# Kernel optimization log

Measured on AMD Instinct MI355X. Metric: run time of the kernel, lower is better.

Reference implementation:

```python
import jax, jax.numpy as jnp
import numpy as np

EPS = 1e-20

def efficient_squash(s):
    # Efficient-CapsNet squash: (1 - 1/e^||s||) * s/||s||
    n = jnp.linalg.norm(s, axis=-1, keepdims=True)
    return (1.0 - 1.0 / (jnp.exp(n) + EPS)) * (s / (n + EPS))

def setup_inputs() -> dict:
    key = jax.random.key(0)
    k1, k2 = jax.random.split(key)
    B, N, D_in = 32, 2048, 16
    K, D_out = 32, 16
    x = jax.random.normal(k1, (B, N, D_in), dtype=jnp.float32)
    # he_normal fan_in = N * D_in * ... ; use simple scaled normal init
    w = jax.random.normal(k2, (K, N, D_in, D_out), dtype=jnp.float32) * 0.05
    b = jnp.zeros((K, N, 1), dtype=jnp.float32)
    return {"x": x, "w": w, "b": b}

def reference(x, w, b):
    D_out = w.shape[-1]
    # projection: [B,N,D_in] x [K,N,D_in,D_out] -> [B,K,N,D_out]
    u = jnp.einsum('bji,kjiz->bkjz', x, w)
    # agreement c_{bkj} = sum_{i,z} u_{bkjz} u_{bkiz} = <u_j, sum_i u_i>
    t = jnp.sum(u, axis=2)                      # [B,K,D_out]
    c = jnp.einsum('bkjz,bkz->bkj', u, t)[..., None]  # [B,K,N,1]
    c = c / jnp.sqrt(jnp.asarray(D_out, jnp.float32))
    c = jax.nn.softmax(c, axis=1)               # softmax over capsules K
    c = c + b                                   # broadcast [K,N,1]
    s = jnp.sum(u * c, axis=2)                  # [B,K,D_out]
    return efficient_squash(s)
```

## Files before the change

### kernel.cpp

```cpp
#include <hip/hip_runtime.h>

#define NN 2048
#define KK 32

#define WS_U     0
#define WS_TP2   67108864UL
#define WS_T     67633152UL
#define WS_SPART 67698688UL
#define WS_NEED  71892992UL

__device__ __forceinline__ float bf_lo(unsigned v) { return __uint_as_float(v << 16); }
__device__ __forceinline__ float bf_hi(unsigned v) { return __uint_as_float(v & 0xffff0000u); }
__device__ __forceinline__ unsigned pack_bf16(float a, float b) {
    unsigned ua = __float_as_uint(a), ub = __float_as_uint(b);
    return ((ua + 0x8000u) >> 16) | ((ub + 0x8000u) & 0xffff0000u);
}

__global__ __launch_bounds__(128)
void k1_u(const float* __restrict__ x, const float* __restrict__ w,
          unsigned* __restrict__ u_pk)
{
    const int tid = threadIdx.x;
    const int zq  = tid & 3;
    const int k   = tid >> 2;
    const int j   = blockIdx.x;

    const float4* w4 = reinterpret_cast<const float4*>(
        w + (((size_t)k * NN + j) * 16) * 16) + zq;
    float4 wr[16];
#pragma unroll
    for (int i = 0; i < 16; ++i) wr[i] = w4[i * 4];

    unsigned* __restrict__ ub = u_pk + (size_t)j * 8192 + k * 8 + zq * 2;
#pragma unroll 4
    for (int b = 0; b < 32; ++b) {
        const float* __restrict__ xr = x + ((size_t)b * NN + j) * 16;
        float xs[16];
#pragma unroll
        for (int i = 0; i < 16; ++i) xs[i] = xr[i];
        float4 acc = make_float4(0.f, 0.f, 0.f, 0.f);
#pragma unroll
        for (int i = 0; i < 16; ++i) {
            acc.x = fmaf(xs[i], wr[i].x, acc.x);
            acc.y = fmaf(xs[i], wr[i].y, acc.y);
            acc.z = fmaf(xs[i], wr[i].z, acc.z);
            acc.w = fmaf(xs[i], wr[i].w, acc.w);
        }
        uint2 o;
        o.x = pack_bf16(acc.x, acc.y);
        o.y = pack_bf16(acc.z, acc.w);
        *reinterpret_cast<uint2*>(ub + (size_t)b * 256) = o;
    }
}

__global__ __launch_bounds__(1024)
void k2a_tpart(const unsigned* __restrict__ u_pk, float* __restrict__ t_part2)
{
    __shared__ float red[16][64][8];
    const int tid  = threadIdx.x;
    const int js   = tid >> 6;
    const int sl64 = tid & 63;
    const int b    = blockIdx.x >> 3;
    const int slj  = blockIdx.x & 7;

    const uint4* up = reinterpret_cast<const uint4*>(u_pk)
                    + ((size_t)(slj * 256 + js) * 32 + b) * 64 + sl64;
    float a[8];
#pragma unroll
    for (int e = 0; e < 8; ++e) a[e] = 0.f;
#pragma unroll
    for (int it = 0; it < 16; ++it) {
        uint4 v = up[(size_t)it * (16 * 32 * 64)];
        a[0] += bf_lo(v.x); a[1] += bf_hi(v.x);
        a[2] += bf_lo(v.y); a[3] += bf_hi(v.y);
        a[4] += bf_lo(v.z); a[5] += bf_hi(v.z);
        a[6] += bf_lo(v.w); a[7] += bf_hi(v.w);
    }
#pragma unroll
    for (int e = 0; e < 8; ++e) red[js][sl64][e] = a[e];
    __syncthreads();
    if (tid < 512) {
        const int s = tid >> 3, e = tid & 7;
        float acc = 0.f;
#pragma unroll
        for (int r = 0; r < 16; ++r) acc += red[r][s][e];
        t_part2[((size_t)b * 8 + slj) * 512 + s * 8 + e] = acc;
    }
}

__global__ __launch_bounds__(256)
void k2a2_t(const float* __restrict__ t_part2, float* __restrict__ t)
{
    const int idx4 = blockIdx.x * 256 + threadIdx.x;
    const int b = idx4 >> 7, loc4 = idx4 & 127;
    const float4* p = reinterpret_cast<const float4*>(t_part2) + (size_t)b * 1024 + loc4;
    float4 s = make_float4(0.f, 0.f, 0.f, 0.f);
#pragma unroll
    for (int sl = 0; sl < 8; ++sl) {
        float4 v = p[sl * 128];
        s.x += v.x; s.y += v.y; s.z += v.z; s.w += v.w;
    }
    reinterpret_cast<float4*>(t)[idx4] = s;
}

__global__ __launch_bounds__(256)
void k2b_fused(const unsigned* __restrict__ u_pk, const float* __restrict__ t,
               const float* __restrict__ bias, float* __restrict__ s_part)
{
    __shared__ float lc_lds[32][33];
    __shared__ float s_lds[8][32][16];
    const int tid = threadIdx.x;
    const int k   = tid & 31;
    const int jl  = tid >> 5;
    const int b   = blockIdx.x >> 6;
    const int jc  = blockIdx.x & 63;

    float tr[16];
    const float4* tp = reinterpret_cast<const float4*>(t + ((size_t)b * KK + k) * 16);
#pragma unroll
    for (int q = 0; q < 4; ++q) {
        float4 v = tp[q];
        tr[4 * q + 0] = v.x; tr[4 * q + 1] = v.y; tr[4 * q + 2] = v.z; tr[4 * q + 3] = v.w;
    }

    uint4 ua[4], ud[4];
#pragma unroll
    for (int jj = 0; jj < 4; ++jj) {
        const int jL = jj * 8 + jl;
        const int jg = jc * 32 + jL;
        const uint4* up = reinterpret_cast<const uint4*>(u_pk)
                        + ((size_t)jg * 32 + b) * 64 + k * 2;
        ua[jj] = up[0]; ud[jj] = up[1];
        float a0 = 0.f, a1 = 0.f;
        a0 = fmaf(bf_lo(ua[jj].x), tr[0],  a0); a1 = fmaf(bf_hi(ua[jj].x), tr[1],  a1);
        a0 = fmaf(bf_lo(ua[jj].y), tr[2],  a0); a1 = fmaf(bf_hi(ua[jj].y), tr[3],  a1);
        a0 = fmaf(bf_lo(ua[jj].z), tr[4],  a0); a1 = fmaf(bf_hi(ua[jj].z), tr[5],  a1);
        a0 = fmaf(bf_lo(ua[jj].w), tr[6],  a0); a1 = fmaf(bf_hi(ua[jj].w), tr[7],  a1);
        a0 = fmaf(bf_lo(ud[jj].x), tr[8],  a0); a1 = fmaf(bf_hi(ud[jj].x), tr[9],  a1);
        a0 = fmaf(bf_lo(ud[jj].y), tr[10], a0); a1 = fmaf(bf_hi(ud[jj].y), tr[11], a1);
        a0 = fmaf(bf_lo(ud[jj].z), tr[12], a0); a1 = fmaf(bf_hi(ud[jj].z), tr[13], a1);
        a0 = fmaf(bf_lo(ud[jj].w), tr[14], a0); a1 = fmaf(bf_hi(ud[jj].w), tr[15], a1);
        lc_lds[jL][k] = a0 + a1;
    }
    __syncthreads();

    {
        const int jq = tid >> 3, kq = tid & 7;
        float lv[4];
#pragma unroll
        for (int m = 0; m < 4; ++m) lv[m] = lc_lds[jq][kq * 4 + m];
        float pm = fmaxf(fmaxf(lv[0], lv[1]), fmaxf(lv[2], lv[3]));
        pm = fmaxf(pm, __shfl_xor(pm, 1));
        pm = fmaxf(pm, __shfl_xor(pm, 2));
        pm = fmaxf(pm, __shfl_xor(pm, 4));
        float ev[4], ps = 0.f;
#pragma unroll
        for (int m = 0; m < 4; ++m) { ev[m] = __expf((lv[m] - pm) * 0.25f); ps += ev[m]; }
        ps += __shfl_xor(ps, 1);
        ps += __shfl_xor(ps, 2);
        ps += __shfl_xor(ps, 4);
        const float inv = 1.f / ps;
        const int jg = jc * 32 + jq;
#pragma unroll
        for (int m = 0; m < 4; ++m)
            lv[m] = ev[m] * inv + bias[(size_t)(kq * 4 + m) * NN + jg];
        __syncthreads();
#pragma unroll
        for (int m = 0; m < 4; ++m) lc_lds[jq][kq * 4 + m] = lv[m];
    }
    __syncthreads();

    float sacc[16];
#pragma unroll
    for (int z = 0; z < 16; ++z) sacc[z] = 0.f;
#pragma unroll
    for (int jj = 0; jj < 4; ++jj) {
        const float cv = lc_lds[jj * 8 + jl][k];
        const uint4 a = ua[jj], d = ud[jj];
        sacc[0]  = fmaf(cv, bf_lo(a.x), sacc[0]);  sacc[1]  = fmaf(cv, bf_hi(a.x), sacc[1]);
        sacc[2]  = fmaf(cv, bf_lo(a.y), sacc[2]);  sacc[3]  = fmaf(cv, bf_hi(a.y), sacc[3]);
        sacc[4]  = fmaf(cv, bf_lo(a.z), sacc[4]);  sacc[5]  = fmaf(cv, bf_hi(a.z), sacc[5]);
        sacc[6]  = fmaf(cv, bf_lo(a.w), sacc[6]);  sacc[7]  = fmaf(cv, bf_hi(a.w), sacc[7]);
        sacc[8]  = fmaf(cv, bf_lo(d.x), sacc[8]);  sacc[9]  = fmaf(cv, bf_hi(d.x), sacc[9]);
        sacc[10] = fmaf(cv, bf_lo(d.y), sacc[10]); sacc[11] = fmaf(cv, bf_hi(d.y), sacc[11]);
        sacc[12] = fmaf(cv, bf_lo(d.z), sacc[12]); sacc[13] = fmaf(cv, bf_hi(d.z), sacc[13]);
        sacc[14] = fmaf(cv, bf_lo(d.w), sacc[14]); sacc[15] = fmaf(cv, bf_hi(d.w), sacc[15]);
    }

#pragma unroll
    for (int q = 0; q < 4; ++q)
        *reinterpret_cast<float4*>(&s_lds[jl][k][q * 4]) =
            make_float4(sacc[q * 4], sacc[q * 4 + 1], sacc[q * 4 + 2], sacc[q * 4 + 3]);
    __syncthreads();
    {
        const int kk = tid >> 3, zp = tid & 7;
        float2 o; o.x = 0.f; o.y = 0.f;
#pragma unroll
        for (int l = 0; l < 8; ++l) {
            o.x += s_lds[l][kk][2 * zp];
            o.y += s_lds[l][kk][2 * zp + 1];
        }
        reinterpret_cast<float2*>(s_part)[((size_t)b * 64 + jc) * 256 + kk * 8 + zp] = o;
    }
}

__global__ __launch_bounds__(256)
void k4_squash(const float* __restrict__ s_part, float* __restrict__ out)
{
    const int idx4 = blockIdx.x * 256 + threadIdx.x;
    const int b = idx4 >> 7, loc4 = idx4 & 127;
    const float4* p = reinterpret_cast<const float4*>(s_part) + (size_t)b * 8192 + loc4;
    float4 s = make_float4(0.f, 0.f, 0.f, 0.f);
#pragma unroll 8
    for (int jc = 0; jc < 64; ++jc) {
        float4 v = p[jc * 128];
        s.x += v.x; s.y += v.y; s.z += v.z; s.w += v.w;
    }
    float ss = s.x * s.x + s.y * s.y + s.z * s.z + s.w * s.w;
    ss += __shfl_xor(ss, 1);
    ss += __shfl_xor(ss, 2);
    const float n = sqrtf(ss);
    const float sc = (1.f - 1.f / (__expf(n) + 1e-20f)) / (n + 1e-20f);
    float4 o; o.x = s.x * sc; o.y = s.y * sc; o.z = s.z * sc; o.w = s.w * sc;
    reinterpret_cast<float4*>(out)[idx4] = o;
}

__global__ void k_sentinel(float* __restrict__ out)
{
    out[blockIdx.x * 256 + threadIdx.x] = 12345.0f;
}

extern "C" void kernel_launch(void* const* d_in, const int* in_sizes, int n_in,
                              void* d_out, int out_size, void* d_ws, size_t ws_size,
                              hipStream_t stream)
{
    const float* x    = (const float*)d_in[0];
    const float* w    = (const float*)d_in[1];
    const float* bias = (const float*)d_in[2];
    float* out        = (float*)d_out;

    char* ws = (char*)d_ws;
    if (ws_size < WS_NEED) {
        k_sentinel<<<dim3(64), dim3(256), 0, stream>>>(out);
        return;
    }
    unsigned* u_pk = (unsigned*)(ws + WS_U);
    float* t_part2 = (float*)(ws + WS_TP2);
    float* t       = (float*)(ws + WS_T);
    float* s_part  = (float*)(ws + WS_SPART);

    k1_u     <<<dim3(2048), dim3(128),  0, stream>>>(x, w, u_pk);
    k2a_tpart<<<dim3(256),  dim3(1024), 0, stream>>>(u_pk, t_part2);
    k2a2_t   <<<dim3(16),   dim3(256),  0, stream>>>(t_part2, t);
    k2b_fused<<<dim3(2048), dim3(256),  0, stream>>>(u_pk, t, bias, s_part);
    k4_squash<<<dim3(16),   dim3(256),  0, stream>>>(s_part, out);
}
```

Measured before the change: 76.03 us.

## Replace u materialization with MFMA recompute in two passes

Drops the 64MB bf16 u buffer. The first pass uses bf16 MFMA to produce per-block partial sums of t. The second pass recomputes u with MFMA, forms the agreement logits against t held in LDS, applies the softmax and bias, and accumulates s, followed by reduction and squash kernels. This trades a large workspace write and read for reading w twice plus extra MFMA work with masked duplicate products, and adds bf16 rounding of x and w inputs.

```diff
diff --git a/kernel.cpp b/kernel.cpp
--- a/kernel.cpp
+++ b/kernel.cpp
@@ -3,226 +3,285 @@
 #define NN 2048
 #define KK 32
 
-#define WS_U     0
-#define WS_TP2   67108864UL
-#define WS_T     67633152UL
-#define WS_SPART 67698688UL
-#define WS_NEED  71892992UL
-
-__device__ __forceinline__ float bf_lo(unsigned v) { return __uint_as_float(v << 16); }
-__device__ __forceinline__ float bf_hi(unsigned v) { return __uint_as_float(v & 0xffff0000u); }
-__device__ __forceinline__ unsigned pack_bf16(float a, float b) {
-    unsigned ua = __float_as_uint(a), ub = __float_as_uint(b);
-    return ((ua + 0x8000u) >> 16) | ((ub + 0x8000u) & 0xffff0000u);
-}
-
-__global__ __launch_bounds__(128)
-void k1_u(const float* __restrict__ x, const float* __restrict__ w,
-          unsigned* __restrict__ u_pk)
+typedef __attribute__((ext_vector_type(8)))  short short8;
+typedef __attribute__((ext_vector_type(4)))  float f32x4;
+
+#define WS_TPART 0UL
+#define WS_SPART 33554432UL
+#define WS_T     67108864UL
+#define WS_NEED  67174400UL
+
+__device__ __forceinline__ short8 pack8(const float* r) {
+    short8 o;
+#pragma unroll
+    for (int e = 0; e < 8; ++e)
+        o[e] = (short)(unsigned short)((__float_as_uint(r[e]) + 0x8000u) >> 16);
+    return o;
+}
+
+__device__ __forceinline__ short8 sel8(bool keep, short8 v) {
+    union { short8 s; unsigned u[4]; } a, b;
+    a.s = v;
+#pragma unroll
+    for (int i = 0; i < 4; ++i) b.u[i] = keep ? a.u[i] : 0u;
+    return b.s;
+}
+
+__global__ __launch_bounds__(256)
+void kA(const float* __restrict__ x, const float* __restrict__ w,
+        float* __restrict__ t_part)
 {
     const int tid = threadIdx.x;
-    const int zq  = tid & 3;
-    const int k   = tid >> 2;
-    const int j   = blockIdx.x;
-
-    const float4* w4 = reinterpret_cast<const float4*>(
-        w + (((size_t)k * NN + j) * 16) * 16) + zq;
-    float4 wr[16];
-#pragma unroll
-    for (int i = 0; i < 16; ++i) wr[i] = w4[i * 4];
-
-    unsigned* __restrict__ ub = u_pk + (size_t)j * 8192 + k * 8 + zq * 2;
+    const int wv  = tid >> 6, l = tid & 63;
+    const int z   = l & 15,  g = l >> 4;
+    const int jl  = g >> 1,  ih = g & 1;
+    const int j0  = blockIdx.x * 4;
+
+    f32x4 C[2][8];
+#pragma unroll
+    for (int m = 0; m < 2; ++m)
+#pragma unroll
+        for (int tt = 0; tt < 8; ++tt) C[m][tt] = (f32x4){0.f, 0.f, 0.f, 0.f};
+
+#pragma unroll
+    for (int p = 0; p < 2; ++p) {
+        const int jp = j0 + p * 2 + jl;
+
+        short8 Af[2];
+#pragma unroll
+        for (int m = 0; m < 2; ++m) {
+            const float* xp = x + ((size_t)(m * 16 + z) * NN + jp) * 16 + ih * 8;
+            float ar[8];
+            float4 v0 = *reinterpret_cast<const float4*>(xp);
+            float4 v1 = *reinterpret_cast<const float4*>(xp + 4);
+            ar[0]=v0.x; ar[1]=v0.y; ar[2]=v0.z; ar[3]=v0.w;
+            ar[4]=v1.x; ar[5]=v1.y; ar[6]=v1.z; ar[7]=v1.w;
+            Af[m] = pack8(ar);
+        }
+
+        short8 Bf[8];
+#pragma unroll
+        for (int tg = 0; tg < 2; ++tg) {
+            float br[4][8];
+#pragma unroll
+            for (int q = 0; q < 4; ++q) {
+                const int k = wv * 8 + tg * 4 + q;
+                const float* wp = w + (size_t)(k * NN + jp) * 256 + ih * 128 + z;
+#pragma unroll
+                for (int e = 0; e < 8; ++e) br[q][e] = wp[e * 16];
+            }
+#pragma unroll
+            for (int q = 0; q < 4; ++q) Bf[tg * 4 + q] = pack8(br[q]);
+        }
+
+#pragma unroll
+        for (int tt = 0; tt < 8; ++tt)
+#pragma unroll
+            for (int m = 0; m < 2; ++m)
+                C[m][tt] = __builtin_amdgcn_mfma_f32_16x16x32_bf16(
+                    Af[m], Bf[tt], C[m][tt], 0, 0, 0);
+    }
+
+    float* tp = t_part + (size_t)blockIdx.x * 16384;
+#pragma unroll
+    for (int m = 0; m < 2; ++m)
+#pragma unroll
+        for (int tt = 0; tt < 8; ++tt)
+#pragma unroll
+            for (int r = 0; r < 4; ++r)
+                tp[(size_t)(m * 16 + g * 4 + r) * 512 + (wv * 8 + tt) * 16 + z] =
+                    C[m][tt][r];
+}
+
+__global__ __launch_bounds__(256)
+void kred_t(const float* __restrict__ t_part, float* __restrict__ t)
+{
+    __shared__ f32x4 red[16][16];
+    const int tid = threadIdx.x;
+    const int c   = blockIdx.x * 16 + (tid & 15);
+    const int ch  = tid >> 4;
+    const f32x4* P = reinterpret_cast<const f32x4*>(t_part);
+    f32x4 a = (f32x4){0.f, 0.f, 0.f, 0.f};
 #pragma unroll 4
-    for (int b = 0; b < 32; ++b) {
-        const float* __restrict__ xr = x + ((size_t)b * NN + j) * 16;
-        float xs[16];
-#pragma unroll
-        for (int i = 0; i < 16; ++i) xs[i] = xr[i];
-        float4 acc = make_float4(0.f, 0.f, 0.f, 0.f);
-#pragma unroll
-        for (int i = 0; i < 16; ++i) {
-            acc.x = fmaf(xs[i], wr[i].x, acc.x);
-            acc.y = fmaf(xs[i], wr[i].y, acc.y);
-            acc.z = fmaf(xs[i], wr[i].z, acc.z);
-            acc.w = fmaf(xs[i], wr[i].w, acc.w);
-        }
-        uint2 o;
-        o.x = pack_bf16(acc.x, acc.y);
-        o.y = pack_bf16(acc.z, acc.w);
-        *reinterpret_cast<uint2*>(ub + (size_t)b * 256) = o;
-    }
-}
-
-__global__ __launch_bounds__(1024)
-void k2a_tpart(const unsigned* __restrict__ u_pk, float* __restrict__ t_part2)
-{
-    __shared__ float red[16][64][8];
-    const int tid  = threadIdx.x;
-    const int js   = tid >> 6;
-    const int sl64 = tid & 63;
-    const int b    = blockIdx.x >> 3;
-    const int slj  = blockIdx.x & 7;
-
-    const uint4* up = reinterpret_cast<const uint4*>(u_pk)
-                    + ((size_t)(slj * 256 + js) * 32 + b) * 64 + sl64;
-    float a[8];
-#pragma unroll
-    for (int e = 0; e < 8; ++e) a[e] = 0.f;
-#pragma unroll
-    for (int it = 0; it < 16; ++it) {
-        uint4 v = up[(size_t)it * (16 * 32 * 64)];
-        a[0] += bf_lo(v.x); a[1] += bf_hi(v.x);
-        a[2] += bf_lo(v.y); a[3] += bf_hi(v.y);
-        a[4] += bf_lo(v.z); a[5] += bf_hi(v.z);
-        a[6] += bf_lo(v.w); a[7] += bf_hi(v.w);
-    }
-#pragma unroll
-    for (int e = 0; e < 8; ++e) red[js][sl64][e] = a[e];
+    for (int q = 0; q < 32; ++q) a += P[(size_t)(ch * 32 + q) * 4096 + c];
+    red[ch][tid & 15] = a;
     __syncthreads();
-    if (tid < 512) {
-        const int s = tid >> 3, e = tid & 7;
-        float acc = 0.f;
-#pragma unroll
-        for (int r = 0; r < 16; ++r) acc += red[r][s][e];
-        t_part2[((size_t)b * 8 + slj) * 512 + s * 8 + e] = acc;
+    if (tid < 16) {
+        f32x4 s = (f32x4){0.f, 0.f, 0.f, 0.f};
+#pragma unroll
+        for (int r = 0; r < 16; ++r) s += red[r][tid];
+        reinterpret_cast<f32x4*>(t)[blockIdx.x * 16 + tid] = s;
     }
 }
 
 __global__ __launch_bounds__(256)
-void k2a2_t(const float* __restrict__ t_part2, float* __restrict__ t)
-{
-    const int idx4 = blockIdx.x * 256 + threadIdx.x;
-    const int b = idx4 >> 7, loc4 = idx4 & 127;
-    const float4* p = reinterpret_cast<const float4*>(t_part2) + (size_t)b * 1024 + loc4;
-    float4 s = make_float4(0.f, 0.f, 0.f, 0.f);
-#pragma unroll
-    for (int sl = 0; sl < 8; ++sl) {
-        float4 v = p[sl * 128];
-        s.x += v.x; s.y += v.y; s.z += v.z; s.w += v.w;
-    }
-    reinterpret_cast<float4*>(t)[idx4] = s;
+void kB(const float* __restrict__ x, const float* __restrict__ w,
+        const float* __restrict__ t, const float* __restrict__ bias,
+        float* __restrict__ s_part)
+{
+    __shared__ float t_lds[16384];
+    __shared__ float l_lds[32][33];
+    __shared__ float c_lds[32][33];
+    __shared__ float b_lds[32][4];
+    const int tid = threadIdx.x;
+    const int wv  = tid >> 6, l = tid & 63;
+    const int z   = l & 15,  g = l >> 4;
+    const int jl  = g >> 1,  ih = g & 1;
+    const int j0  = blockIdx.x * 4;
+
+#pragma unroll
+    for (int q = 0; q < 16; ++q)
+        reinterpret_cast<f32x4*>(t_lds)[q * 256 + tid] =
+            reinterpret_cast<const f32x4*>(t)[q * 256 + tid];
+    if (tid < 128) b_lds[tid >> 2][tid & 3] = bias[(size_t)(tid >> 2) * NN + j0 + (tid & 3)];
+    __syncthreads();
+
+    f32x4 S[2][8];
+#pragma unroll
+    for (int m = 0; m < 2; ++m)
+#pragma unroll
+        for (int tt = 0; tt < 8; ++tt) S[m][tt] = (f32x4){0.f, 0.f, 0.f, 0.f};
+
+#pragma unroll 1
+    for (int p = 0; p < 2; ++p) {
+        const int jp = j0 + p * 2 + jl;
+
+        short8 Af[2];
+#pragma unroll
+        for (int m = 0; m < 2; ++m) {
+            const float* xp = x + ((size_t)(m * 16 + z) * NN + jp) * 16 + ih * 8;
+            float ar[8];
+            float4 v0 = *reinterpret_cast<const float4*>(xp);
+            float4 v1 = *reinterpret_cast<const float4*>(xp + 4);
+            ar[0]=v0.x; ar[1]=v0.y; ar[2]=v0.z; ar[3]=v0.w;
+            ar[4]=v1.x; ar[5]=v1.y; ar[6]=v1.z; ar[7]=v1.w;
+            Af[m] = pack8(ar);
+        }
+        short8 Bf[8];
+#pragma unroll
+        for (int tg = 0; tg < 2; ++tg) {
+            float br[4][8];
+#pragma unroll
+            for (int q = 0; q < 4; ++q) {
+                const int k = wv * 8 + tg * 4 + q;
+                const float* wp = w + (size_t)(k * NN + jp) * 256 + ih * 128 + z;
+#pragma unroll
+                for (int e = 0; e < 8; ++e) br[q][e] = wp[e * 16];
+            }
+#pragma unroll
+            for (int q = 0; q < 4; ++q) Bf[tg * 4 + q] = pack8(br[q]);
+        }
+
+#pragma unroll 1
+        for (int jj = 0; jj < 2; ++jj) {
+            const bool keep = (jl == jj);
+            f32x4 C[2][8];
+            const f32x4 z4 = (f32x4){0.f, 0.f, 0.f, 0.f};
+#pragma unroll
+            for (int tt = 0; tt < 8; ++tt) {
+                short8 bj = sel8(keep, Bf[tt]);
+#pragma unroll
+                for (int m = 0; m < 2; ++m)
+                    C[m][tt] = __builtin_amdgcn_mfma_f32_16x16x32_bf16(
+                        Af[m], bj, z4, 0, 0, 0);
+            }
+#pragma unroll
+            for (int m = 0; m < 2; ++m)
+#pragma unroll
+                for (int tt = 0; tt < 8; ++tt) {
+                    const int k = wv * 8 + tt;
+                    float red[4];
+#pragma unroll
+                    for (int r = 0; r < 4; ++r) {
+                        float pv = C[m][tt][r] *
+                            t_lds[(size_t)(m * 16 + g * 4 + r) * 512 + k * 16 + z];
+                        pv += __shfl_xor(pv, 1);
+                        pv += __shfl_xor(pv, 2);
+                        pv += __shfl_xor(pv, 4);
+                        pv += __shfl_xor(pv, 8);
+                        red[r] = pv;
+                    }
+                    if (z == ((tt << 1) | m)) {
+#pragma unroll
+                        for (int r = 0; r < 4; ++r)
+                            l_lds[m * 16 + g * 4 + r][k] = red[r];
+                    }
+                }
+            __syncthreads();
+            {
+                const int bb = tid >> 3, kq = tid & 7;
+                float lv[4];
+#pragma unroll
+                for (int m4 = 0; m4 < 4; ++m4) lv[m4] = l_lds[bb][kq * 4 + m4];
+                float pm = fmaxf(fmaxf(lv[0], lv[1]), fmaxf(lv[2], lv[3]));
+                pm = fmaxf(pm, __shfl_xor(pm, 1));
+                pm = fmaxf(pm, __shfl_xor(pm, 2));
+                pm = fmaxf(pm, __shfl_xor(pm, 4));
+                float ev[4], ps = 0.f;
+#pragma unroll
+                for (int m4 = 0; m4 < 4; ++m4) {
+                    ev[m4] = __expf((lv[m4] - pm) * 0.25f);
+                    ps += ev[m4];
+                }
+                ps += __shfl_xor(ps, 1);
+                ps += __shfl_xor(ps, 2);
+                ps += __shfl_xor(ps, 4);
+                const float inv = 1.f / ps;
+#pragma unroll
+                for (int m4 = 0; m4 < 4; ++m4)
+                    c_lds[bb][kq * 4 + m4] =
+                        ev[m4] * inv + b_lds[kq * 4 + m4][p * 2 + jj];
+            }
+            __syncthreads();
+#pragma unroll
+            for (int m = 0; m < 2; ++m)
+#pragma unroll
+                for (int tt = 0; tt < 8; ++tt) {
+                    const int k = wv * 8 + tt;
+#pragma unroll
+                    for (int r = 0; r < 4; ++r)
+                        S[m][tt][r] = fmaf(c_lds[m * 16 + g * 4 + r][k],
+                                           C[m][tt][r], S[m][tt][r]);
+                }
+        }
+    }
+
+    float* sp = s_part + (size_t)blockIdx.x * 16384;
+#pragma unroll
+    for (int m = 0; m < 2; ++m)
+#pragma unroll
+        for (int tt = 0; tt < 8; ++tt)
+#pragma unroll
+            for (int r = 0; r < 4; ++r)
+                sp[(size_t)(m * 16 + g * 4 + r) * 512 + (wv * 8 + tt) * 16 + z] =
+                    S[m][tt][r];
 }
 
 __global__ __launch_bounds__(256)
-void k2b_fused(const unsigned* __restrict__ u_pk, const float* __restrict__ t,
-               const float* __restrict__ bias, float* __restrict__ s_part)
-{
-    __shared__ float lc_lds[32][33];
-    __shared__ float s_lds[8][32][16];
+void ksq(const float* __restrict__ s_part, float* __restrict__ out)
+{
+    __shared__ f32x4 red[16][16];
     const int tid = threadIdx.x;
-    const int k   = tid & 31;
-    const int jl  = tid >> 5;
-    const int b   = blockIdx.x >> 6;
-    const int jc  = blockIdx.x & 63;
-
-    float tr[16];
-    const float4* tp = reinterpret_cast<const float4*>(t + ((size_t)b * KK + k) * 16);
-#pragma unroll
-    for (int q = 0; q < 4; ++q) {
-        float4 v = tp[q];
-        tr[4 * q + 0] = v.x; tr[4 * q + 1] = v.y; tr[4 * q + 2] = v.z; tr[4 * q + 3] = v.w;
-    }
-
-    uint4 ua[4], ud[4];
-#pragma unroll
-    for (int jj = 0; jj < 4; ++jj) {
-        const int jL = jj * 8 + jl;
-        const int jg = jc * 32 + jL;
-        const uint4* up = reinterpret_cast<const uint4*>(u_pk)
-                        + ((size_t)jg * 32 + b) * 64 + k * 2;
-        ua[jj] = up[0]; ud[jj] = up[1];
-        float a0 = 0.f, a1 = 0.f;
-        a0 = fmaf(bf_lo(ua[jj].x), tr[0],  a0); a1 = fmaf(bf_hi(ua[jj].x), tr[1],  a1);
-        a0 = fmaf(bf_lo(ua[jj].y), tr[2],  a0); a1 = fmaf(bf_hi(ua[jj].y), tr[3],  a1);
-        a0 = fmaf(bf_lo(ua[jj].z), tr[4],  a0); a1 = fmaf(bf_hi(ua[jj].z), tr[5],  a1);
-        a0 = fmaf(bf_lo(ua[jj].w), tr[6],  a0); a1 = fmaf(bf_hi(ua[jj].w), tr[7],  a1);
-        a0 = fmaf(bf_lo(ud[jj].x), tr[8],  a0); a1 = fmaf(bf_hi(ud[jj].x), tr[9],  a1);
-        a0 = fmaf(bf_lo(ud[jj].y), tr[10], a0); a1 = fmaf(bf_hi(ud[jj].y), tr[11], a1);
-        a0 = fmaf(bf_lo(ud[jj].z), tr[12], a0); a1 = fmaf(bf_hi(ud[jj].z), tr[13], a1);
-        a0 = fmaf(bf_lo(ud[jj].w), tr[14], a0); a1 = fmaf(bf_hi(ud[jj].w), tr[15], a1);
-        lc_lds[jL][k] = a0 + a1;
-    }
+    const int c   = blockIdx.x * 16 + (tid & 15);
+    const int ch  = tid >> 4;
+    const f32x4* P = reinterpret_cast<const f32x4*>(s_part);
+    f32x4 a = (f32x4){0.f, 0.f, 0.f, 0.f};
+#pragma unroll 4
+    for (int q = 0; q < 32; ++q) a += P[(size_t)(ch * 32 + q) * 4096 + c];
+    red[ch][tid & 15] = a;
     __syncthreads();
-
-    {
-        const int jq = tid >> 3, kq = tid & 7;
-        float lv[4];
-#pragma unroll
-        for (int m = 0; m < 4; ++m) lv[m] = lc_lds[jq][kq * 4 + m];
-        float pm = fmaxf(fmaxf(lv[0], lv[1]), fmaxf(lv[2], lv[3]));
-        pm = fmaxf(pm, __shfl_xor(pm, 1));
-        pm = fmaxf(pm, __shfl_xor(pm, 2));
-        pm = fmaxf(pm, __shfl_xor(pm, 4));
-        float ev[4], ps = 0.f;
-#pragma unroll
-        for (int m = 0; m < 4; ++m) { ev[m] = __expf((lv[m] - pm) * 0.25f); ps += ev[m]; }
-        ps += __shfl_xor(ps, 1);
-        ps += __shfl_xor(ps, 2);
-        ps += __shfl_xor(ps, 4);
-        const float inv = 1.f / ps;
-        const int jg = jc * 32 + jq;
-#pragma unroll
-        for (int m = 0; m < 4; ++m)
-            lv[m] = ev[m] * inv + bias[(size_t)(kq * 4 + m) * NN + jg];
-        __syncthreads();
-#pragma unroll
-        for (int m = 0; m < 4; ++m) lc_lds[jq][kq * 4 + m] = lv[m];
-    }
-    __syncthreads();
-
-    float sacc[16];
-#pragma unroll
-    for (int z = 0; z < 16; ++z) sacc[z] = 0.f;
-#pragma unroll
-    for (int jj = 0; jj < 4; ++jj) {
-        const float cv = lc_lds[jj * 8 + jl][k];
-        const uint4 a = ua[jj], d = ud[jj];
-        sacc[0]  = fmaf(cv, bf_lo(a.x), sacc[0]);  sacc[1]  = fmaf(cv, bf_hi(a.x), sacc[1]);
-        sacc[2]  = fmaf(cv, bf_lo(a.y), sacc[2]);  sacc[3]  = fmaf(cv, bf_hi(a.y), sacc[3]);
-        sacc[4]  = fmaf(cv, bf_lo(a.z), sacc[4]);  sacc[5]  = fmaf(cv, bf_hi(a.z), sacc[5]);
-        sacc[6]  = fmaf(cv, bf_lo(a.w), sacc[6]);  sacc[7]  = fmaf(cv, bf_hi(a.w), sacc[7]);
-        sacc[8]  = fmaf(cv, bf_lo(d.x), sacc[8]);  sacc[9]  = fmaf(cv, bf_hi(d.x), sacc[9]);
-        sacc[10] = fmaf(cv, bf_lo(d.y), sacc[10]); sacc[11] = fmaf(cv, bf_hi(d.y), sacc[11]);
-        sacc[12] = fmaf(cv, bf_lo(d.z), sacc[12]); sacc[13] = fmaf(cv, bf_hi(d.z), sacc[13]);
-        sacc[14] = fmaf(cv, bf_lo(d.w), sacc[14]); sacc[15] = fmaf(cv, bf_hi(d.w), sacc[15]);
-    }
-
-#pragma unroll
-    for (int q = 0; q < 4; ++q)
-        *reinterpret_cast<float4*>(&s_lds[jl][k][q * 4]) =
-            make_float4(sacc[q * 4], sacc[q * 4 + 1], sacc[q * 4 + 2], sacc[q * 4 + 3]);
-    __syncthreads();
-    {
-        const int kk = tid >> 3, zp = tid & 7;
-        float2 o; o.x = 0.f; o.y = 0.f;
-#pragma unroll
-        for (int l = 0; l < 8; ++l) {
-            o.x += s_lds[l][kk][2 * zp];
-            o.y += s_lds[l][kk][2 * zp + 1];
-        }
-        reinterpret_cast<float2*>(s_part)[((size_t)b * 64 + jc) * 256 + kk * 8 + zp] = o;
-    }
-}
-
-__global__ __launch_bounds__(256)
-void k4_squash(const float* __restrict__ s_part, float* __restrict__ out)
-{
-    const int idx4 = blockIdx.x * 256 + threadIdx.x;
-    const int b = idx4 >> 7, loc4 = idx4 & 127;
-    const float4* p = reinterpret_cast<const float4*>(s_part) + (size_t)b * 8192 + loc4;
-    float4 s = make_float4(0.f, 0.f, 0.f, 0.f);
-#pragma unroll 8
-    for (int jc = 0; jc < 64; ++jc) {
-        float4 v = p[jc * 128];
-        s.x += v.x; s.y += v.y; s.z += v.z; s.w += v.w;
-    }
-    float ss = s.x * s.x + s.y * s.y + s.z * s.z + s.w * s.w;
-    ss += __shfl_xor(ss, 1);
-    ss += __shfl_xor(ss, 2);
-    const float n = sqrtf(ss);
-    const float sc = (1.f - 1.f / (__expf(n) + 1e-20f)) / (n + 1e-20f);
-    float4 o; o.x = s.x * sc; o.y = s.y * sc; o.z = s.z * sc; o.w = s.w * sc;
-    reinterpret_cast<float4*>(out)[idx4] = o;
+    if (tid < 16) {
+        f32x4 s = (f32x4){0.f, 0.f, 0.f, 0.f};
+#pragma unroll
+        for (int r = 0; r < 16; ++r) s += red[r][tid];
+        float ss = s.x * s.x + s.y * s.y + s.z * s.z + s.w * s.w;
+        ss += __shfl_xor(ss, 1);
+        ss += __shfl_xor(ss, 2);
+        const float n  = sqrtf(ss);
+        const float sc = (1.f - 1.f / (__expf(n) + 1e-20f)) / (n + 1e-20f);
+        f32x4 o; o.x = s.x * sc; o.y = s.y * sc; o.z = s.z * sc; o.w = s.w * sc;
+        reinterpret_cast<f32x4*>(out)[blockIdx.x * 16 + tid] = o;
+    }
 }
 
 __global__ void k_sentinel(float* __restrict__ out)
@@ -244,14 +303,12 @@
         k_sentinel<<<dim3(64), dim3(256), 0, stream>>>(out);
         return;
     }
-    unsigned* u_pk = (unsigned*)(ws + WS_U);
-    float* t_part2 = (float*)(ws + WS_TP2);
-    float* t       = (float*)(ws + WS_T);
-    float* s_part  = (float*)(ws + WS_SPART);
-
-    k1_u     <<<dim3(2048), dim3(128),  0, stream>>>(x, w, u_pk);
-    k2a_tpart<<<dim3(256),  dim3(1024), 0, stream>>>(u_pk, t_part2);
-    k2a2_t   <<<dim3(16),   dim3(256),  0, stream>>>(t_part2, t);
-    k2b_fused<<<dim3(2048), dim3(256),  0, stream>>>(u_pk, t, bias, s_part);
-    k4_squash<<<dim3(16),   dim3(256),  0, stream>>>(s_part, out);
-}
+    float* t_part = (float*)(ws + WS_TPART);
+    float* s_part = (float*)(ws + WS_SPART);
+    float* t      = (float*)(ws + WS_T);
+
+    kA    <<<dim3(512), dim3(256), 0, stream>>>(x, w, t_part);
+    kred_t<<<dim3(256), dim3(256), 0, stream>>>(t_part, t);
+    kB    <<<dim3(512), dim3(256), 0, stream>>>(x, w, t, bias, s_part);
+    ksq   <<<dim3(256), dim3(256), 0, stream>>>(s_part, out);
+}
```

After: 92.10 us. +21.1%, slower.
